# Performance work log

Hardware: AMD Instinct MI355X
Metric: run time of the kernel (lower is better)

## Reference

```python
import jax, jax.numpy as jnp
import numpy as np
from jax import lax

CAPACITY = 32768
KEY_SIZE = 64
VALUE_SIZE = 64
BATCH = 4096


def setup_inputs() -> dict:
    key = jax.random.key(0)
    ks = jax.random.split(key, 9)
    inp = {
        "keys": jax.random.normal(ks[0], (BATCH, KEY_SIZE), dtype=jnp.float32),
        "values": jax.random.normal(ks[1], (BATCH, VALUE_SIZE), dtype=jnp.float32),
        "query": jax.random.normal(ks[2], (BATCH, KEY_SIZE), dtype=jnp.float32),
        # learned memory tables (init as torch.randn * 0.01)
        "mem_keys": jax.random.normal(ks[3], (CAPACITY, KEY_SIZE), dtype=jnp.float32) * 0.01,
        "mem_values": jax.random.normal(ks[4], (CAPACITY, VALUE_SIZE), dtype=jnp.float32) * 0.01,
        # nn.Linear params (fan-in uniform init approximation)
        "Wk": jax.random.uniform(ks[5], (KEY_SIZE, KEY_SIZE), jnp.float32, -1, 1) / np.sqrt(KEY_SIZE),
        "bk": jax.random.uniform(ks[6], (KEY_SIZE,), jnp.float32, -1, 1) / np.sqrt(KEY_SIZE),
        "Wv": jax.random.uniform(ks[7], (VALUE_SIZE, VALUE_SIZE), jnp.float32, -1, 1) / np.sqrt(VALUE_SIZE),
        "bv": jax.random.uniform(ks[8], (VALUE_SIZE,), jnp.float32, -1, 1) / np.sqrt(VALUE_SIZE),
    }
    return inp


def reference(keys, values, query, mem_keys, mem_values, Wk, bk, Wv, bv):
    # NOTE: forward() calls self.store(keys, query): `query` is stored as the
    # values, and the `values` arg is never used. Reproduced faithfully.
    batch = keys.shape[0]
    capacity = mem_keys.shape[0]

    # ---- store ----
    keys_proj = jnp.tanh(keys @ Wk.T + bk)                      # [B, K]
    sim = keys_proj @ mem_keys.T                                # [B, cap] (big)
    # argmax of softmax == argmax of logits
    top_match = jnp.argmax(sim, axis=-1)                        # [B]
    stored_vals = jnp.tanh(query @ Wv.T + bv)                   # [B, V]

    # matching the sequential Python loop in the original.
    winner = jnp.full((capacity,), -1, dtype=jnp.int32).at[top_match].max(
        jnp.arange(batch, dtype=jnp.int32))                     # [cap]
    written = (winner >= 0)[:, None]
    safe_winner = jnp.clip(winner, 0, batch - 1)
    # .detach() in original -> stop_gradient on written entries
    new_keys = jnp.where(written, lax.stop_gradient(keys_proj)[safe_winner], mem_keys)
    new_values = jnp.where(written, lax.stop_gradient(stored_vals)[safe_winner], mem_values)

    # ---- retrieve ----
    query_proj = jnp.tanh(query @ Wk.T + bk)                    # [B, K]
    attention = jax.nn.softmax(query_proj @ new_keys.T, axis=-1)  # [B, cap]
    retrieved = attention @ new_values                          # [B, V]
    return retrieved, attention
```

## Files before the change

kernel.cpp:

```cpp
#include <hip/hip_runtime.h>
#include <math.h>
#include <float.h>

#define BATCH 4096
#define CAP   32768

typedef _Float16 f16;
typedef _Float16 f16x8 __attribute__((ext_vector_type(8)));
typedef float    f32x4 __attribute__((ext_vector_type(4)));

__device__ __forceinline__ f32x4 MF(f16x8 a, f16x8 b, f32x4 c) {
    return __builtin_amdgcn_mfma_f32_16x16x32_f16(a, b, c, 0, 0, 0);
}

__global__ __launch_bounds__(256) void prep_kernel(
    const float* __restrict__ keys, const float* __restrict__ query,
    const float* __restrict__ Wk, const float* __restrict__ bk,
    const float* __restrict__ Wv, const float* __restrict__ bv,
    const float* __restrict__ mk,
    f16* __restrict__ kph, f16* __restrict__ kpl,
    f16* __restrict__ svh,
    f16* __restrict__ qph, f16* __restrict__ qpl,
    f16* __restrict__ mkh, f16* __restrict__ mkl,
    int* __restrict__ winner)
{
    int bx = blockIdx.x;
    int tid = threadIdx.x;
    if (bx >= 768) {
        int i = (bx - 768)*256 + tid;
        float x = mk[i];
        f16 h = (f16)x;
        mkh[i] = h;
        mkl[i] = (f16)((x - (float)h) * 2048.0f);
        if (i < CAP) winner[i] = -1;
        return;
    }
    int job = bx >> 8;
    const float *in, *W, *b; f16 *oh, *ol; bool scaled;
    if (job == 0)      { in = keys;  W = Wk; b = bk; oh = kph; ol = kpl;     scaled = true;  }
    else if (job == 1) { in = query; W = Wv; b = bv; oh = svh; ol = nullptr; scaled = false; }
    else               { in = query; W = Wk; b = bk; oh = qph; ol = qpl;     scaled = false; }

    __shared__ float Wl[64*65];
    __shared__ float inl[16*65];
    __shared__ float bl[64];
    int row0 = (bx & 255) * 16;
    for (int i = tid; i < 4096; i += 256) { int r = i >> 6, c = i & 63; Wl[r*65+c] = W[i]; }
    for (int i = tid; i < 1024; i += 256) { int r = i >> 6, c = i & 63; inl[r*65+c] = in[(row0+r)*64 + c]; }
    if (tid < 64) bl[tid] = b[tid];
    __syncthreads();

    int col = tid & 63;
    int rq  = tid >> 6;
    #pragma unroll
    for (int q = 0; q < 4; ++q) {
        int r = rq*4 + q;
        float acc = bl[col];
        #pragma unroll
        for (int k = 0; k < 64; ++k) acc += inl[r*65+k] * Wl[col*65+k];
        float t = tanhf(acc);
        f16 h = (f16)t;
        oh[(row0+r)*64 + col] = h;
        if (ol) {
            float lo = t - (float)h;
            if (scaled) lo *= 2048.0f;
            ol[(row0+r)*64 + col] = (f16)lo;
        }
    }
}

__global__ __launch_bounds__(256, 2) void sim_kernel(
    const f16* __restrict__ Aph, const f16* __restrict__ Apl,
    const f16* __restrict__ Bph, const f16* __restrict__ Bpl,
    float* __restrict__ bestv, int* __restrict__ besti)
{
    __shared__ __align__(16) f16 Bh[64*72], Bl[64*72];
    int tid = threadIdx.x, l = tid & 63, w = tid >> 6;
    int sb = blockIdx.x, rb = blockIdx.y;
    int row0 = rb*256 + w*64;
    int lr = l & 15, lg = l >> 4;
    int sl0 = tid >> 3, ch = tid & 7;

    f16x8 ah[4][2], al[4][2];
    #pragma unroll
    for (int i = 0; i < 4; ++i)
        #pragma unroll
        for (int t = 0; t < 2; ++t) {
            size_t o = (size_t)(row0 + i*16 + lr)*64 + t*32 + lg*8;
            ah[i][t] = *(const f16x8*)&Aph[o];
            al[i][t] = *(const f16x8*)&Apl[o];
        }
    float bvv[4][4]; int bii[4][4];
    #pragma unroll
    for (int i = 0; i < 4; ++i)
        #pragma unroll
        for (int j = 0; j < 4; ++j) { bvv[i][j] = -FLT_MAX; bii[i][j] = 0; }

    f16x8 pb[2][2];
    {
        int s0 = sb*1024;
        pb[0][0] = *(const f16x8*)&Bph[(size_t)(s0+sl0)*64 + ch*8];
        pb[0][1] = *(const f16x8*)&Bpl[(size_t)(s0+sl0)*64 + ch*8];
        pb[1][0] = *(const f16x8*)&Bph[(size_t)(s0+sl0+32)*64 + ch*8];
        pb[1][1] = *(const f16x8*)&Bpl[(size_t)(s0+sl0+32)*64 + ch*8];
    }

    for (int st = 0; st < 16; ++st) {
        int s0 = sb*1024 + st*64;
        __syncthreads();
        *(f16x8*)&Bh[sl0*72 + ch*8]      = pb[0][0];
        *(f16x8*)&Bl[sl0*72 + ch*8]      = pb[0][1];
        *(f16x8*)&Bh[(sl0+32)*72 + ch*8] = pb[1][0];
        *(f16x8*)&Bl[(sl0+32)*72 + ch*8] = pb[1][1];
        __syncthreads();
        if (st + 1 < 16) {
            int sn = s0 + 64;
            pb[0][0] = *(const f16x8*)&Bph[(size_t)(sn+sl0)*64 + ch*8];
            pb[0][1] = *(const f16x8*)&Bpl[(size_t)(sn+sl0)*64 + ch*8];
            pb[1][0] = *(const f16x8*)&Bph[(size_t)(sn+sl0+32)*64 + ch*8];
            pb[1][1] = *(const f16x8*)&Bpl[(size_t)(sn+sl0+32)*64 + ch*8];
        }
        #pragma unroll
        for (int cf = 0; cf < 4; ++cf) {
            int c0 = cf*16;
            f16x8 bh[2], bl2[2];
            #pragma unroll
            for (int t = 0; t < 2; ++t) {
                bh[t]  = *(const f16x8*)&Bh[(c0+lr)*72 + t*32 + lg*8];
                bl2[t] = *(const f16x8*)&Bl[(c0+lr)*72 + t*32 + lg*8];
            }
            f32x4 z = {0.f,0.f,0.f,0.f};
            f32x4 aA[4] = {z,z,z,z}, aB[4] = {z,z,z,z};
            #pragma unroll
            for (int i = 0; i < 4; ++i)
                #pragma unroll
                for (int t = 0; t < 2; ++t) {
                    aA[i] = MF(ah[i][t], bh[t],  aA[i]);
                    aB[i] = MF(ah[i][t], bl2[t], aB[i]);
                    aB[i] = MF(al[i][t], bh[t],  aB[i]);
                }
            int slot = s0 + c0 + lr;
            #pragma unroll
            for (int i = 0; i < 4; ++i)
                #pragma unroll
                for (int j = 0; j < 4; ++j) {
                    float v = aA[i][j] + aB[i][j]*(1.0f/2048.0f);
                    if (v > bvv[i][j]) { bvv[i][j] = v; bii[i][j] = slot; }
                }
        }
    }
    #pragma unroll
    for (int m = 1; m < 16; m <<= 1)
        #pragma unroll
        for (int i = 0; i < 4; ++i)
            #pragma unroll
            for (int j = 0; j < 4; ++j) {
                float ov = __shfl_xor(bvv[i][j], m);
                int   oi = __shfl_xor(bii[i][j], m);
                if (ov > bvv[i][j] || (ov == bvv[i][j] && oi < bii[i][j])) { bvv[i][j] = ov; bii[i][j] = oi; }
            }
    if (lr == 0) {
        #pragma unroll
        for (int i = 0; i < 4; ++i)
            #pragma unroll
            for (int j = 0; j < 4; ++j) {
                int r = row0 + i*16 + lg*4 + j;
                bestv[r*32 + sb] = bvv[i][j];
                besti[r*32 + sb] = bii[i][j];
            }
    }
}

__global__ void argmax_scatter_kernel(const float* __restrict__ bestv,
                                      const int* __restrict__ besti,
                                      int* __restrict__ winner)
{
    int r = blockIdx.x*256 + threadIdx.x;
    if (r >= BATCH) return;
    float bv = bestv[r*32]; int bi = besti[r*32];
    #pragma unroll
    for (int sb = 1; sb < 32; ++sb) {
        float v = bestv[r*32+sb]; int ii = besti[r*32+sb];
        if (v > bv || (v == bv && ii < bi)) { bv = v; bi = ii; }
    }
    atomicMax(&winner[bi], r);
}

__global__ __launch_bounds__(256) void build_kernel(
    const int* __restrict__ winner,
    const f16* __restrict__ kph, const f16* __restrict__ kpl,
    const f16* __restrict__ svh,
    const float* __restrict__ mk, const float* __restrict__ mv,
    f16* __restrict__ nkh, f16* __restrict__ nkl,
    f16* __restrict__ nvTh)
{
    __shared__ __align__(16) f16 Lh[64*72];
    int tid = threadIdx.x;
    int s0 = blockIdx.x*64;
    #pragma unroll
    for (int c = 0; c < 2; ++c) {
        int task = tid + 256*c; int sl = task >> 3, ch = task & 7;
        int s = s0 + sl; int w = winner[s];
        f16x8 hk, lk, hv;
        if (w >= 0) {
            hk = *(const f16x8*)&kph[(size_t)w*64 + ch*8];
            f16x8 lraw = *(const f16x8*)&kpl[(size_t)w*64 + ch*8];
            #pragma unroll
            for (int q = 0; q < 8; ++q) lk[q] = (f16)((float)lraw[q] * (1.0f/2048.0f));
            hv = *(const f16x8*)&svh[(size_t)w*64 + ch*8];
        } else {
            #pragma unroll
            for (int q = 0; q < 8; ++q) {
                float x = mk[(size_t)s*64 + ch*8 + q];
                f16 h = (f16)x; hk[q] = h; lk[q] = (f16)(x - (float)h);
                float y = mv[(size_t)s*64 + ch*8 + q];
                hv[q] = (f16)y;
            }
        }
        *(f16x8*)&nkh[(size_t)s*64 + ch*8] = hk;
        *(f16x8*)&nkl[(size_t)s*64 + ch*8] = lk;
        *(f16x8*)&Lh[sl*72 + ch*8] = hv;
    }
    __syncthreads();
    int v = tid >> 2, sc = (tid & 3)*16;
    f16x8 a, b2;
    #pragma unroll
    for (int q = 0; q < 8; ++q) { a[q] = Lh[(sc+q)*72 + v]; b2[q] = Lh[(sc+8+q)*72 + v]; }
    *(f16x8*)&nvTh[(size_t)v*CAP + s0 + sc]     = a;
    *(f16x8*)&nvTh[(size_t)v*CAP + s0 + sc + 8] = b2;
}

__global__ __launch_bounds__(256, 2) void logits_stats_kernel(
    const f16* __restrict__ Aph,
    const f16* __restrict__ Bph,
    float* __restrict__ s_part)
{
    __shared__ __align__(16) f16 Bh[64*72];
    int tid = threadIdx.x, l = tid & 63, w = tid >> 6;
    int sb = blockIdx.x, rb = blockIdx.y;
    int row0 = rb*512 + w*128;
    int lr = l & 15, lg = l >> 4;
    int sl0 = tid >> 3, ch = tid & 7;

    f16x8 ah[8][2];
    #pragma unroll
    for (int i = 0; i < 8; ++i)
        #pragma unroll
        for (int t = 0; t < 2; ++t)
            ah[i][t] = *(const f16x8*)&Aph[(size_t)(row0 + i*16 + lr)*64 + t*32 + lg*8];

    float ssum[8][4];
    #pragma unroll
    for (int i = 0; i < 8; ++i)
        #pragma unroll
        for (int j = 0; j < 4; ++j) ssum[i][j] = 0.f;

    f16x8 pb[2];
    {
        int s0 = sb*512;
        pb[0] = *(const f16x8*)&Bph[(size_t)(s0+sl0)*64 + ch*8];
        pb[1] = *(const f16x8*)&Bph[(size_t)(s0+sl0+32)*64 + ch*8];
    }

    for (int st = 0; st < 8; ++st) {
        int s0 = sb*512 + st*64;
        __syncthreads();
        *(f16x8*)&Bh[sl0*72 + ch*8]      = pb[0];
        *(f16x8*)&Bh[(sl0+32)*72 + ch*8] = pb[1];
        __syncthreads();
        if (st + 1 < 8) {
            int sn = s0 + 64;
            pb[0] = *(const f16x8*)&Bph[(size_t)(sn+sl0)*64 + ch*8];
            pb[1] = *(const f16x8*)&Bph[(size_t)(sn+sl0+32)*64 + ch*8];
        }
        #pragma unroll
        for (int cf = 0; cf < 4; ++cf) {
            int c0 = cf*16;
            f16x8 bh[2];
            #pragma unroll
            for (int t = 0; t < 2; ++t)
                bh[t] = *(const f16x8*)&Bh[(c0+lr)*72 + t*32 + lg*8];
            f32x4 z = {0.f,0.f,0.f,0.f};
            f32x4 acc[8] = {z,z,z,z,z,z,z,z};
            #pragma unroll
            for (int i = 0; i < 8; ++i) {
                acc[i] = MF(ah[i][0], bh[0], acc[i]);
                acc[i] = MF(ah[i][1], bh[1], acc[i]);
            }
            #pragma unroll
            for (int i = 0; i < 8; ++i)
                #pragma unroll
                for (int j = 0; j < 4; ++j)
                    ssum[i][j] += __expf(acc[i][j]);
        }
    }
    #pragma unroll
    for (int m = 1; m < 16; m <<= 1)
        #pragma unroll
        for (int i = 0; i < 8; ++i)
            #pragma unroll
            for (int j = 0; j < 4; ++j)
                ssum[i][j] += __shfl_xor(ssum[i][j], m);
    if (lr == 0) {
        #pragma unroll
        for (int i = 0; i < 8; ++i)
            #pragma unroll
            for (int j = 0; j < 4; ++j) {
                int r = row0 + i*16 + lg*4 + j;
                s_part[r*64 + sb] = ssum[i][j];
            }
    }
}

__global__ __launch_bounds__(256, 2) void pass2_kernel(
    const f16* __restrict__ qph, const f16* __restrict__ qpl,
    const f16* __restrict__ nkh, const f16* __restrict__ nkl,
    const f16* __restrict__ nvTh,
    const float* __restrict__ s_part,
    float* __restrict__ att, float* __restrict__ ret_part)
{
    __shared__ __align__(16) f16 Kh[64*72], Kl[64*72];
    __shared__ __align__(16) f16 Vh[64*72];
    __shared__ __align__(16) f16 Ph[128*72];
    __shared__ float iSl[128];
    int tid = threadIdx.x, l = tid & 63, w = tid >> 6;
    int wr = w >> 1, wc = w & 1;
    int sb = blockIdx.x, rb = blockIdx.y;
    int wrow0 = rb*128 + wr*64;
    int lr = l & 15, lg = l >> 4;
    int sl0 = tid >> 3, ch = tid & 7;

    {
        int r_loc = tid >> 1, half = tid & 1;
        const float4* p = (const float4*)(s_part + (size_t)(rb*128 + r_loc)*64 + half*32);
        float S = 0.f;
        #pragma unroll
        for (int q = 0; q < 8; ++q) {
            float4 v = p[q];
            S += (v.x + v.y) + (v.z + v.w);
        }
        S += __shfl_xor(S, 1);
        if (!half) iSl[r_loc] = 1.0f / S;
    }

    f16x8 ah[4][2], al[4][2];
    #pragma unroll
    for (int i = 0; i < 4; ++i)
        #pragma unroll
        for (int t = 0; t < 2; ++t) {
            size_t o = (size_t)(wrow0 + i*16 + lr)*64 + t*32 + lg*8;
            ah[i][t] = *(const f16x8*)&qph[o];
            al[i][t] = *(const f16x8*)&qpl[o];
        }
    f16x8 pk[2][2], pv[2];
    {
        int s0g = sb*2048;
        pk[0][0] = *(const f16x8*)&nkh[(size_t)(s0g+sl0)*64 + ch*8];
        pk[0][1] = *(const f16x8*)&nkl[(size_t)(s0g+sl0)*64 + ch*8];
        pk[1][0] = *(const f16x8*)&nkh[(size_t)(s0g+sl0+32)*64 + ch*8];
        pk[1][1] = *(const f16x8*)&nkl[(size_t)(s0g+sl0+32)*64 + ch*8];
        pv[0]    = *(const f16x8*)&nvTh[(size_t)sl0*CAP + s0g + ch*8];
        pv[1]    = *(const f16x8*)&nvTh[(size_t)(sl0+32)*CAP + s0g + ch*8];
    }
    __syncthreads();
    float iS[4][4];
    #pragma unroll
    for (int i = 0; i < 4; ++i)
        #pragma unroll
        for (int j = 0; j < 4; ++j)
            iS[i][j] = iSl[wr*64 + i*16 + lg*4 + j];

    f32x4 z = {0.f,0.f,0.f,0.f};
    f32x4 pacc[4][2] = {{z,z},{z,z},{z,z},{z,z}};

    for (int st = 0; st < 32; ++st) {
        int s0g = sb*2048 + st*64;
        __syncthreads();
        *(f16x8*)&Kh[sl0*72 + ch*8]      = pk[0][0];
        *(f16x8*)&Kl[sl0*72 + ch*8]      = pk[0][1];
        *(f16x8*)&Kh[(sl0+32)*72 + ch*8] = pk[1][0];
        *(f16x8*)&Kl[(sl0+32)*72 + ch*8] = pk[1][1];
        *(f16x8*)&Vh[sl0*72 + ch*8]      = pv[0];
        *(f16x8*)&Vh[(sl0+32)*72 + ch*8] = pv[1];
        __syncthreads();
        if (st + 1 < 32) {
            int sn = s0g + 64;
            pk[0][0] = *(const f16x8*)&nkh[(size_t)(sn+sl0)*64 + ch*8];
            pk[0][1] = *(const f16x8*)&nkl[(size_t)(sn+sl0)*64 + ch*8];
            pk[1][0] = *(const f16x8*)&nkh[(size_t)(sn+sl0+32)*64 + ch*8];
            pk[1][1] = *(const f16x8*)&nkl[(size_t)(sn+sl0+32)*64 + ch*8];
            pv[0]    = *(const f16x8*)&nvTh[(size_t)sl0*CAP + sn + ch*8];
            pv[1]    = *(const f16x8*)&nvTh[(size_t)(sl0+32)*CAP + sn + ch*8];
        }
        #pragma unroll
        for (int cf = 0; cf < 2; ++cf) {
            int c0 = wc*32 + cf*16;
            f16x8 bh[2], bl2[2];
            #pragma unroll
            for (int t = 0; t < 2; ++t) {
                bh[t]  = *(const f16x8*)&Kh[(c0+lr)*72 + t*32 + lg*8];
                bl2[t] = *(const f16x8*)&Kl[(c0+lr)*72 + t*32 + lg*8];
            }
            f32x4 qacc[4] = {z,z,z,z};
            #pragma unroll
            for (int i = 0; i < 4; ++i)
                #pragma unroll
                for (int t = 0; t < 2; ++t) {
                    qacc[i] = MF(ah[i][t], bh[t],  qacc[i]);
                    qacc[i] = MF(ah[i][t], bl2[t], qacc[i]);
                    qacc[i] = MF(al[i][t], bh[t],  qacc[i]);
                }
            #pragma unroll
            for (int i = 0; i < 4; ++i)
                #pragma unroll
                for (int j = 0; j < 4; ++j) {
                    float a = __expf(qacc[i][j]) * iS[i][j];
                    Ph[(wr*64 + i*16 + lg*4 + j)*72 + c0 + lr] = (f16)a;
                }
        }
        __syncthreads();
        f16x8 pah[4][2];
        #pragma unroll
        for (int i = 0; i < 4; ++i)
            #pragma unroll
            for (int t = 0; t < 2; ++t)
                pah[i][t] = *(const f16x8*)&Ph[(wr*64 + i*16 + lr)*72 + t*32 + lg*8];
        #pragma unroll
        for (int vf = 0; vf < 2; ++vf) {
            f16x8 vbh[2];
            #pragma unroll
            for (int t = 0; t < 2; ++t)
                vbh[t] = *(const f16x8*)&Vh[(wc*32 + vf*16 + lr)*72 + t*32 + lg*8];
            #pragma unroll
            for (int i = 0; i < 4; ++i)
                #pragma unroll
                for (int t = 0; t < 2; ++t)
                    pacc[i][vf] = MF(pah[i][t], vbh[t], pacc[i][vf]);
        }
        #pragma unroll
        for (int it = 0; it < 4; ++it) {
            int rloc = it*32 + (tid >> 3);
            int k0 = (tid & 7)*8;
            f16x8 ph = *(const f16x8*)&Ph[rloc*72 + k0];
            f32x4 lo = {(float)ph[0], (float)ph[1], (float)ph[2], (float)ph[3]};
            f32x4 hi = {(float)ph[4], (float)ph[5], (float)ph[6], (float)ph[7]};
            float* dst = &att[(size_t)(rb*128 + rloc)*CAP + s0g + k0];
            *(f32x4*)dst = lo;
            *(f32x4*)(dst + 4) = hi;
        }
    }
    #pragma unroll
    for (int i = 0; i < 4; ++i)
        #pragma unroll
        for (int vf = 0; vf < 2; ++vf)
            #pragma unroll
            for (int j = 0; j < 4; ++j) {
                int gr = wrow0 + i*16 + lg*4 + j;
                int gc = wc*32 + vf*16 + lr;
                ret_part[((size_t)sb*BATCH + gr)*64 + gc] = pacc[i][vf][j];
            }
}

__global__ void ret_reduce_kernel(const float* __restrict__ rp, float* __restrict__ out)
{
    int i4 = blockIdx.x*256 + threadIdx.x;
    float4 s = {0.f,0.f,0.f,0.f};
    #pragma unroll
    for (int sb = 0; sb < 16; ++sb) {
        float4 p = ((const float4*)(rp + (size_t)sb*BATCH*64))[i4];
        s.x += p.x; s.y += p.y; s.z += p.z; s.w += p.w;
    }
    ((float4*)out)[i4] = s;
}

extern "C" void kernel_launch(void* const* d_in, const int* in_sizes, int n_in,
                              void* d_out, int out_size, void* d_ws, size_t ws_size,
                              hipStream_t stream) {
    const float* keys       = (const float*)d_in[0];
    const float* query      = (const float*)d_in[2];
    const float* mem_keys   = (const float*)d_in[3];
    const float* mem_values = (const float*)d_in[4];
    const float* Wk         = (const float*)d_in[5];
    const float* bk         = (const float*)d_in[6];
    const float* Wv         = (const float*)d_in[7];
    const float* bv         = (const float*)d_in[8];

    float* out = (float*)d_out;
    float* ret = out;
    float* att = out + BATCH*64;

    char* ws = (char*)d_ws;
    const size_t SK = (size_t)BATCH*64*2;
    const size_t SC = (size_t)CAP*64*2;
    f16* kph  = (f16*)(ws + 0*SK);
    f16* kpl  = (f16*)(ws + 1*SK);
    f16* svh  = (f16*)(ws + 2*SK);
    f16* qph  = (f16*)(ws + 3*SK);
    f16* qpl  = (f16*)(ws + 4*SK);
    size_t o = 5*SK;
    f16* nkh  = (f16*)(ws + o);            o += SC;
    f16* nkl  = (f16*)(ws + o);            o += SC;
    f16* nvTh = (f16*)(ws + o);            o += SC;
    float* bestv  = (float*)(ws + o);      o += (size_t)BATCH*32*4;
    int*   besti  = (int*)(ws + o);        o += (size_t)BATCH*32*4;
    float* s_part = (float*)(ws + o);      o += (size_t)BATCH*64*4;
    int*   winner = (int*)(ws + o);        o += (size_t)CAP*4;
    float* ret_part = (float*)(ws + o);
    f16* mkh = (f16*)ret_part;
    f16* mkl = (f16*)((char*)ret_part + SC);

    prep_kernel<<<768 + CAP*64/256, 256, 0, stream>>>(
        keys, query, Wk, bk, Wv, bv, mem_keys,
        kph, kpl, svh, qph, qpl, mkh, mkl, winner);
    sim_kernel<<<dim3(32, 16), 256, 0, stream>>>(kph, kpl, mkh, mkl, bestv, besti);
    argmax_scatter_kernel<<<BATCH/256, 256, 0, stream>>>(bestv, besti, winner);
    build_kernel<<<CAP/64, 256, 0, stream>>>(
        winner, kph, kpl, svh, mem_keys, mem_values, nkh, nkl, nvTh);
    logits_stats_kernel<<<dim3(64, 8), 256, 0, stream>>>(qph, nkh, s_part);
    pass2_kernel<<<dim3(16, 32), 256, 0, stream>>>(
        qph, qpl, nkh, nkl, nvTh, s_part, att, ret_part);
    ret_reduce_kernel<<<BATCH*64/4/256, 256, 0, stream>>>(ret_part, ret);
}
```

Before: 328.9 us.

## Give each wave a private P tile in pass2, dropping the block barrier

```diff
diff --git a/kernel.cpp b/kernel.cpp
--- a/kernel.cpp
+++ b/kernel.cpp
@@ -321,26 +321,25 @@
 {
     __shared__ __align__(16) f16 Kh[64*72], Kl[64*72];
     __shared__ __align__(16) f16 Vh[64*72];
-    __shared__ __align__(16) f16 Ph[128*72];
-    __shared__ float iSl[128];
+    __shared__ __align__(16) f16 Ph[4][64*72];
+    __shared__ float iSl[256];
     int tid = threadIdx.x, l = tid & 63, w = tid >> 6;
-    int wr = w >> 1, wc = w & 1;
     int sb = blockIdx.x, rb = blockIdx.y;
-    int wrow0 = rb*128 + wr*64;
+    int brow0 = rb*256;
+    int wrow0 = brow0 + w*64;
     int lr = l & 15, lg = l >> 4;
     int sl0 = tid >> 3, ch = tid & 7;
+    f16* Pw = &Ph[w][0];
 
     {
-        int r_loc = tid >> 1, half = tid & 1;
-        const float4* p = (const float4*)(s_part + (size_t)(rb*128 + r_loc)*64 + half*32);
+        const float4* p = (const float4*)(s_part + (size_t)(brow0 + tid)*64);
         float S = 0.f;
         #pragma unroll
-        for (int q = 0; q < 8; ++q) {
+        for (int q = 0; q < 16; ++q) {
             float4 v = p[q];
             S += (v.x + v.y) + (v.z + v.w);
         }
-        S += __shfl_xor(S, 1);
-        if (!half) iSl[r_loc] = 1.0f / S;
+        iSl[tid] = 1.0f / S;
     }
 
     f16x8 ah[4][2], al[4][2];
@@ -354,7 +353,7 @@
         }
     f16x8 pk[2][2], pv[2];
     {
-        int s0g = sb*2048;
+        int s0g = sb*1024;
         pk[0][0] = *(const f16x8*)&nkh[(size_t)(s0g+sl0)*64 + ch*8];
         pk[0][1] = *(const f16x8*)&nkl[(size_t)(s0g+sl0)*64 + ch*8];
         pk[1][0] = *(const f16x8*)&nkh[(size_t)(s0g+sl0+32)*64 + ch*8];
@@ -368,13 +367,13 @@
     for (int i = 0; i < 4; ++i)
         #pragma unroll
         for (int j = 0; j < 4; ++j)
-            iS[i][j] = iSl[wr*64 + i*16 + lg*4 + j];
+            iS[i][j] = iSl[w*64 + i*16 + lg*4 + j];
 
     f32x4 z = {0.f,0.f,0.f,0.f};
-    f32x4 pacc[4][2] = {{z,z},{z,z},{z,z},{z,z}};
-
-    for (int st = 0; st < 32; ++st) {
-        int s0g = sb*2048 + st*64;
+    f32x4 pacc[4][4] = {{z,z,z,z},{z,z,z,z},{z,z,z,z},{z,z,z,z}};
+
+    for (int st = 0; st < 16; ++st) {
+        int s0g = sb*1024 + st*64;
         __syncthreads();
         *(f16x8*)&Kh[sl0*72 + ch*8]      = pk[0][0];
         *(f16x8*)&Kl[sl0*72 + ch*8]      = pk[0][1];
@@ -383,7 +382,7 @@
         *(f16x8*)&Vh[sl0*72 + ch*8]      = pv[0];
         *(f16x8*)&Vh[(sl0+32)*72 + ch*8] = pv[1];
         __syncthreads();
-        if (st + 1 < 32) {
+        if (st + 1 < 16) {
             int sn = s0g + 64;
             pk[0][0] = *(const f16x8*)&nkh[(size_t)(sn+sl0)*64 + ch*8];
             pk[0][1] = *(const f16x8*)&nkl[(size_t)(sn+sl0)*64 + ch*8];
@@ -393,8 +392,8 @@
             pv[1]    = *(const f16x8*)&nvTh[(size_t)(sl0+32)*CAP + sn + ch*8];
         }
         #pragma unroll
-        for (int cf = 0; cf < 2; ++cf) {
-            int c0 = wc*32 + cf*16;
+        for (int cf = 0; cf < 4; ++cf) {
+            int c0 = cf*16;
             f16x8 bh[2], bl2[2];
             #pragma unroll
             for (int t = 0; t < 2; ++t) {
@@ -415,22 +414,22 @@
                 #pragma unroll
                 for (int j = 0; j < 4; ++j) {
                     float a = __expf(qacc[i][j]) * iS[i][j];
-                    Ph[(wr*64 + i*16 + lg*4 + j)*72 + c0 + lr] = (f16)a;
+                    Pw[(i*16 + lg*4 + j)*72 + c0 + lr] = (f16)a;
                 }
         }
-        __syncthreads();
+        asm volatile("s_waitcnt lgkmcnt(0)" ::: "memory");
         f16x8 pah[4][2];
         #pragma unroll
         for (int i = 0; i < 4; ++i)
             #pragma unroll
             for (int t = 0; t < 2; ++t)
-                pah[i][t] = *(const f16x8*)&Ph[(wr*64 + i*16 + lr)*72 + t*32 + lg*8];
-        #pragma unroll
-        for (int vf = 0; vf < 2; ++vf) {
+                pah[i][t] = *(const f16x8*)&Pw[(i*16 + lr)*72 + t*32 + lg*8];
+        #pragma unroll
+        for (int vf = 0; vf < 4; ++vf) {
             f16x8 vbh[2];
             #pragma unroll
             for (int t = 0; t < 2; ++t)
-                vbh[t] = *(const f16x8*)&Vh[(wc*32 + vf*16 + lr)*72 + t*32 + lg*8];
+                vbh[t] = *(const f16x8*)&Vh[(vf*16 + lr)*72 + t*32 + lg*8];
             #pragma unroll
             for (int i = 0; i < 4; ++i)
                 #pragma unroll
@@ -438,13 +437,13 @@
                     pacc[i][vf] = MF(pah[i][t], vbh[t], pacc[i][vf]);
         }
         #pragma unroll
-        for (int it = 0; it < 4; ++it) {
-            int rloc = it*32 + (tid >> 3);
-            int k0 = (tid & 7)*8;
-            f16x8 ph = *(const f16x8*)&Ph[rloc*72 + k0];
+        for (int it = 0; it < 8; ++it) {
+            int rloc = it*8 + (l >> 3);
+            int k0 = (l & 7)*8;
+            f16x8 ph = *(const f16x8*)&Pw[rloc*72 + k0];
             f32x4 lo = {(float)ph[0], (float)ph[1], (float)ph[2], (float)ph[3]};
             f32x4 hi = {(float)ph[4], (float)ph[5], (float)ph[6], (float)ph[7]};
-            float* dst = &att[(size_t)(rb*128 + rloc)*CAP + s0g + k0];
+            float* dst = &att[(size_t)(wrow0 + rloc)*CAP + s0g + k0];
             *(f32x4*)dst = lo;
             *(f32x4*)(dst + 4) = hi;
         }
@@ -452,11 +451,11 @@
     #pragma unroll
     for (int i = 0; i < 4; ++i)
         #pragma unroll
-        for (int vf = 0; vf < 2; ++vf)
+        for (int vf = 0; vf < 4; ++vf)
             #pragma unroll
             for (int j = 0; j < 4; ++j) {
                 int gr = wrow0 + i*16 + lg*4 + j;
-                int gc = wc*32 + vf*16 + lr;
+                int gc = vf*16 + lr;
                 ret_part[((size_t)sb*BATCH + gr)*64 + gc] = pacc[i][vf][j];
             }
 }
@@ -466,7 +465,7 @@
     int i4 = blockIdx.x*256 + threadIdx.x;
     float4 s = {0.f,0.f,0.f,0.f};
     #pragma unroll
-    for (int sb = 0; sb < 16; ++sb) {
+    for (int sb = 0; sb < 32; ++sb) {
         float4 p = ((const float4*)(rp + (size_t)sb*BATCH*64))[i4];
         s.x += p.x; s.y += p.y; s.z += p.z; s.w += p.w;
     }
@@ -517,7 +516,7 @@
     build_kernel<<<CAP/64, 256, 0, stream>>>(
         winner, kph, kpl, svh, mem_keys, mem_values, nkh, nkl, nvTh);
     logits_stats_kernel<<<dim3(64, 8), 256, 0, stream>>>(qph, nkh, s_part);
-    pass2_kernel<<<dim3(16, 32), 256, 0, stream>>>(
+    pass2_kernel<<<dim3(32, 16), 256, 0, stream>>>(
         qph, qpl, nkh, nkl, nvTh, s_part, att, ret_part);
     ret_reduce_kernel<<<BATCH*64/4/256, 256, 0, stream>>>(ret_part, ret);
 }
```

Result: faster. 308.1 us (-6.3%).
